# Performance work log

Hardware: AMD Instinct MI355X
Metric: run time of the kernel (lower is better)

## Reference

```python
import jax, jax.numpy as jnp
import numpy as np

N = 100000
E = 1600000
NIN = 128
NOUT = 128


def setup_inputs() -> dict:
    key = jax.random.key(0)
    k1, k2, k3, k4 = jax.random.split(key, 4)
    x = jax.random.normal(k1, (N, NIN), dtype=jnp.float32)
    edge_index = jax.random.randint(k2, (2, E), 0, N, dtype=jnp.int64)
    edge_attr = jnp.ones((E,), dtype=jnp.float32)  # unused by GCNConv
    # PyG Linear weight is [out, in]; glorot-ish init
    W = jax.random.normal(k3, (NOUT, NIN), dtype=jnp.float32) / np.sqrt(NIN)
    b = jnp.zeros((NOUT,), dtype=jnp.float32)
    return {"x": x, "edge_index": edge_index, "edge_attr": edge_attr, "W": W, "b": b}


def reference(x, edge_index, edge_attr, W, b):
    # PyG GCNConv: add self-loops, symmetric degree normalization,
    # linear transform, scatter-add aggregation at destination, + bias.
    n = x.shape[0]
    loops = jnp.arange(n, dtype=edge_index.dtype)
    src = jnp.concatenate([edge_index[0], loops])  # [E+N]
    dst = jnp.concatenate([edge_index[1], loops])  # [E+N]
    # degree over destination (col) including self-loops, edge weight = 1
    deg = jax.ops.segment_sum(jnp.ones_like(dst, dtype=x.dtype), dst, num_segments=n)
    dinv = jnp.where(deg > 0, jax.lax.rsqrt(deg), 0.0)
    norm = dinv[src] * dinv[dst]  # [E+N]
    h = x @ W.T  # [N, NOUT]
    msg = h[src] * norm[:, None]  # [E+N, NOUT]
    out = jax.ops.segment_sum(msg, dst, num_segments=n)  # [N, NOUT]
    return out + b
```

## Files before the change

### kernel.cpp

```cpp
#include <hip/hip_runtime.h>

#define TPB 256
#define NBLK 256
#define BSH 8
#define BCAP 6144

typedef __attribute__((ext_vector_type(4))) float f32x4;
typedef __attribute__((ext_vector_type(8))) short short8;

__device__ __forceinline__ unsigned short f2bf(float f) {
    unsigned u = __float_as_uint(f);
    u = (u + 0x7fffu + ((u >> 16) & 1u)) >> 16;
    return (unsigned short)u;
}
__device__ __forceinline__ float bflo(unsigned u) { return __uint_as_float(u << 16); }
__device__ __forceinline__ float bfhi(unsigned u) { return __uint_as_float(u & 0xffff0000u); }


__global__ __launch_bounds__(256) void k_scatgemm(
    const int* __restrict__ src, const int* __restrict__ dst,
    int* __restrict__ bcur, unsigned* __restrict__ packed,
    const float* __restrict__ x, const float* __restrict__ W,
    unsigned short* __restrict__ g, int N, int E)
{
    __shared__ __align__(16) char smem[34816];
    const int t = threadIdx.x;

    if (blockIdx.x < NBLK) {
        int* sh = (int*)smem;
        sh[t] = 0; sh[t + 256] = 0;
        __syncthreads();
        int chunk = (E + NBLK - 1) / NBLK;
        int lo = blockIdx.x * chunk;
        int hi = min(E, lo + chunk);
        for (int e = lo + t; e < hi; e += 256)
            atomicAdd(&sh[dst[e] >> BSH], 1);
        __syncthreads();
        int c0 = sh[t], c1 = sh[t + 256];
        int b0 = c0 ? atomicAdd(&bcur[t],       c0) : 0;
        int b1 = c1 ? atomicAdd(&bcur[t + 256], c1) : 0;
        __syncthreads();
        sh[t]       = t * BCAP + b0;
        sh[t + 256] = (t + 256) * BCAP + b1;
        __syncthreads();
        for (int e = lo + t; e < hi; e += 256) {
            int d = dst[e];
            int bkt = d >> BSH;
            int pos = atomicAdd(&sh[bkt], 1);
            if (pos < bkt * BCAP + BCAP)
                packed[pos] = ((unsigned)src[e] << 8) | (unsigned)(d & 255);
        }
    } else {
        typedef unsigned short wb_t[136];
        wb_t* wb = (wb_t*)smem;

        for (int ch = t; ch < 2048; ch += 256) {
            int nrow = ch >> 4, k8 = (ch & 15) << 3;
            const float* wp = W + nrow * 128 + k8;
            float4 w0 = *(const float4*)wp;
            float4 w1 = *(const float4*)(wp + 4);
            union { unsigned short u[8]; uint4 q; } pk;
            pk.u[0] = f2bf(w0.x); pk.u[1] = f2bf(w0.y); pk.u[2] = f2bf(w0.z); pk.u[3] = f2bf(w0.w);
            pk.u[4] = f2bf(w1.x); pk.u[5] = f2bf(w1.y); pk.u[6] = f2bf(w1.z); pk.u[7] = f2bf(w1.w);
            *(uint4*)&wb[nrow][k8] = pk.q;
        }
        __syncthreads();

        const int lane = t & 63;
        const int wid  = t >> 6;
        const int l15  = lane & 15;
        const int quad = lane >> 4;
        const int row  = (blockIdx.x - NBLK) * 64 + wid * 16 + l15;
        const int rowc = (row < N) ? row : (N - 1);

        f32x4 acc[8];
        #pragma unroll
        for (int u = 0; u < 8; ++u) acc[u] = (f32x4){0.f, 0.f, 0.f, 0.f};

        #pragma unroll
        for (int ks = 0; ks < 4; ++ks) {
            const int kb = ks * 32 + quad * 8;
            float4 a0 = *(const float4*)(x + (long)rowc * 128 + kb);
            float4 a1 = *(const float4*)(x + (long)rowc * 128 + kb + 4);
            union { unsigned short u[8]; short8 v; } af;
            af.u[0] = f2bf(a0.x); af.u[1] = f2bf(a0.y); af.u[2] = f2bf(a0.z); af.u[3] = f2bf(a0.w);
            af.u[4] = f2bf(a1.x); af.u[5] = f2bf(a1.y); af.u[6] = f2bf(a1.z); af.u[7] = f2bf(a1.w);
            #pragma unroll
            for (int u = 0; u < 8; ++u) {
                short8 bf = *(const short8*)&wb[u * 16 + l15][kb];
                acc[u] = __builtin_amdgcn_mfma_f32_16x16x32_bf16(bf, af.v, acc[u], 0, 0, 0);
            }
        }

        if (row < N) {
            unsigned short* gp = g + (long)row * 128 + quad * 4;
            #pragma unroll
            for (int u = 0; u < 8; ++u) {
                unsigned short u0 = f2bf(acc[u][0]);
                unsigned short u1 = f2bf(acc[u][1]);
                unsigned short u2 = f2bf(acc[u][2]);
                unsigned short u3 = f2bf(acc[u][3]);
                uint2 pk;
                pk.x = (unsigned)u0 | ((unsigned)u1 << 16);
                pk.y = (unsigned)u2 | ((unsigned)u3 << 16);
                *(uint2*)(gp + u * 16) = pk;
            }
        }
    }
}


__global__ __launch_bounds__(256) void k_bcsr(const unsigned* __restrict__ packed,
                                              const int* __restrict__ bcur,
                                              int* __restrict__ offsets,
                                              int* __restrict__ sorted_src,
                                              float* __restrict__ dinv, int N, int E, int NB) {
    __shared__ int tp0[256], tp1[256];
    __shared__ int bb[513];
    __shared__ int hist[256];
    __shared__ int scur[256];
    __shared__ unsigned stage[BCAP];
    int t = threadIdx.x;

    {
        int v0 = bcur[2 * t], v1 = bcur[2 * t + 1];
        int p = v0 + v1;
        tp0[t] = p;
        __syncthreads();
        int sb = 0;
        for (int d = 1; d < 256; d <<= 1) {
            int* cur = sb ? tp1 : tp0;
            int* nxt = sb ? tp0 : tp1;
            int val = cur[t] + ((t >= d) ? cur[t - d] : 0);
            nxt[t] = val;
            sb ^= 1;
            __syncthreads();
        }
        int* fin = sb ? tp1 : tp0;
        int base = fin[t] - p;
        bb[2 * t] = base;
        bb[2 * t + 1] = base + v0;
        if (t == 0) bb[512] = E;
        __syncthreads();
    }

    for (int b = blockIdx.x; b < NB; b += NBLK) {
        int cnt = min(bcur[b], BCAP);
        int s0g = b * BCAP;
        int o0  = bb[b];
        hist[t] = 0;
        __syncthreads();
        for (int e = t; e < cnt; e += 256)
            atomicAdd(&hist[packed[s0g + e] & 255u], 1);
        __syncthreads();
        int v = hist[t];
        tp0[t] = v;
        __syncthreads();
        int sb = 0;
        for (int d = 1; d < 256; d <<= 1) {
            int* cur = sb ? tp1 : tp0;
            int* nxt = sb ? tp0 : tp1;
            int val = cur[t] + ((t >= d) ? cur[t - d] : 0);
            nxt[t] = val;
            sb ^= 1;
            __syncthreads();
        }
        int* fin = sb ? tp1 : tp0;
        int lbase = fin[t] - v;
        scur[t] = lbase;
        int d = (b << BSH) + t;
        if (d < N) { offsets[d] = o0 + lbase; dinv[d] = rsqrtf((float)v + 1.0f); }
        if (b == 0 && t == 0) offsets[N] = E;
        __syncthreads();
        for (int e = t; e < cnt; e += 256) {
            unsigned pk = packed[s0g + e];
            int pos = atomicAdd(&scur[pk & 255u], 1);
            stage[pos] = pk >> 8;
        }
        __syncthreads();
        for (int i = t; i < cnt; i += 256)
            sorted_src[o0 + i] = (int)stage[i];
        __syncthreads();
    }
}


__global__ __launch_bounds__(256) void k_aggregate(const int* __restrict__ sorted_src,
                                                   const int* __restrict__ offsets,
                                                   const unsigned short* __restrict__ g,
                                                   const float* __restrict__ dinv,
                                                   const float* __restrict__ b,
                                                   float* __restrict__ out, int n) {
    int d = blockIdx.x * (TPB / 32) + (threadIdx.x >> 5);
    if (d >= n) return;
    int c = (threadIdx.x & 31) << 2;
    const char* gb = (const char*)g + (c << 1);

    int s0 = offsets[d];
    int s1 = offsets[d + 1];

    float4 acc = make_float4(0.f, 0.f, 0.f, 0.f);
    auto addrow = [&](int r) {
        float dv = dinv[r];
        uint2 p = *(const uint2*)(gb + (r << 8));
        acc.x = fmaf(bflo(p.x), dv, acc.x);
        acc.y = fmaf(bfhi(p.x), dv, acc.y);
        acc.z = fmaf(bflo(p.y), dv, acc.z);
        acc.w = fmaf(bfhi(p.y), dv, acc.w);
    };

    addrow(d);
    int e = s0;
    for (; e + 8 <= s1; e += 8) {
        int a[8];
        #pragma unroll
        for (int j = 0; j < 8; ++j) a[j] = sorted_src[e + j];
        #pragma unroll
        for (int j = 0; j < 8; ++j) addrow(a[j]);
    }
    for (; e + 4 <= s1; e += 4) {
        int a[4];
        #pragma unroll
        for (int j = 0; j < 4; ++j) a[j] = sorted_src[e + j];
        #pragma unroll
        for (int j = 0; j < 4; ++j) addrow(a[j]);
    }
    for (; e < s1; ++e) addrow(sorted_src[e]);

    float s = dinv[d];
    float4 bb = *(const float4*)(b + c);
    float4 r = make_float4(acc.x * s + bb.x, acc.y * s + bb.y,
                           acc.z * s + bb.z, acc.w * s + bb.w);
    *(float4*)(out + (long)d * 128 + c) = r;
}


extern "C" void kernel_launch(void* const* d_in, const int* in_sizes, int n_in,
                              void* d_out, int out_size, void* d_ws, size_t ws_size,
                              hipStream_t stream) {
    const float* x  = (const float*)d_in[0];
    const int*   ei = (const int*)d_in[1];
    const float* W  = (const float*)d_in[3];
    const float* b  = (const float*)d_in[4];
    float* out = (float*)d_out;

    const int N = in_sizes[0] / 128;
    const int E = in_sizes[1] / 2;
    const int* src = ei;
    const int* dst = ei + E;
    const int NB = (N + 255) >> BSH;

    char* p = (char*)d_ws;
    auto carve = [&](size_t bytes) { char* q = p; p += (bytes + 255) & ~(size_t)255; return q; };
    int*            bcur       = (int*)           carve(512 * 4);
    int*            offsets    = (int*)           carve((size_t)(N + 1) * 4);
    float*          dinv       = (float*)         carve((size_t)N * 4);
    int*            sorted_src = (int*)           carve((size_t)E * 4);
    unsigned*       packed     = (unsigned*)      carve((size_t)512 * BCAP * 4);
    unsigned short* g          = (unsigned short*)carve((size_t)N * 128 * 2);

    const int gemmBlocks = (N + 63) / 64;

    hipMemsetAsync(bcur, 0, 512 * 4, stream);

    k_scatgemm<<<NBLK + gemmBlocks, TPB, 0, stream>>>(src, dst, bcur, packed,
                                                      x, W, g, N, E);
    k_bcsr    <<<NBLK, TPB, 0, stream>>>(packed, bcur, offsets, sorted_src,
                                         dinv, N, E, NB);
    k_aggregate<<<(N + (TPB / 32) - 1) / (TPB / 32), TPB, 0, stream>>>(
        sorted_src, offsets, g, dinv, b, out, N);
}
```

Measured before the change: 231.7 us.

## Restage scatter with LDS-local sort, fuse CSR build into GEMM kernel, prescale rows

The bucket scatter now runs as its own kernel. Each block sorts its edge chunk into buckets in LDS and then writes packed entries contiguously, where before each edge did a scattered global write. Degrees come from global atomics, so the CSR-building pass moves into the GEMM kernel with one block per bucket. The GEMM output is prescaled by the source dinv, which lets aggregation do plain adds on precomputed byte offsets instead of a per-edge dinv gather. The cost is one extra global atomic per edge for the degree count, and the GEMM now has to wait for the scatter kernel instead of overlapping with it.

```diff
diff --git a/kernel.cpp b/kernel.cpp
--- a/kernel.cpp
+++ b/kernel.cpp
@@ -2,8 +2,10 @@
 
 #define TPB 256
 #define NBLK 256
+#define SCTPB 512
 #define BSH 8
 #define BCAP 6144
+#define CHCAP 6272
 
 typedef __attribute__((ext_vector_type(4))) float f32x4;
 typedef __attribute__((ext_vector_type(8))) short short8;
@@ -17,39 +19,143 @@
 __device__ __forceinline__ float bfhi(unsigned u) { return __uint_as_float(u & 0xffff0000u); }
 
 
-__global__ __launch_bounds__(256) void k_scatgemm(
+__global__ __launch_bounds__(SCTPB) void k_scat(
     const int* __restrict__ src, const int* __restrict__ dst,
-    int* __restrict__ bcur, unsigned* __restrict__ packed,
+    int* __restrict__ deg, int* __restrict__ bcur,
+    unsigned* __restrict__ packed, int E)
+{
+    __shared__ int hist[512], lbase[512], lcur[512], gbase[512];
+    __shared__ int tp[2][512];
+    __shared__ unsigned stage[CHCAP];
+    __shared__ unsigned short bktid[CHCAP];
+    const int t = threadIdx.x;
+
+    hist[t] = 0;
+    __syncthreads();
+
+    const int chunk = (E + NBLK - 1) / NBLK;
+    const int lo = blockIdx.x * chunk;
+    const int hi = min(E, lo + chunk);
+
+    for (int e = lo + t; e < hi; e += SCTPB) {
+        int d = dst[e];
+        atomicAdd(&deg[d], 1);
+        atomicAdd(&hist[d >> BSH], 1);
+    }
+    __syncthreads();
+
+    int v = hist[t];
+    tp[0][t] = v;
+    __syncthreads();
+    int sb = 0;
+    for (int dl = 1; dl < 512; dl <<= 1) {
+        int val = tp[sb][t] + ((t >= dl) ? tp[sb][t - dl] : 0);
+        tp[sb ^ 1][t] = val;
+        sb ^= 1;
+        __syncthreads();
+    }
+    int lb = tp[sb][t] - v;
+    lbase[t] = lb;
+    lcur[t]  = lb;
+    gbase[t] = v ? atomicAdd(&bcur[t], v) : 0;
+    __syncthreads();
+
+    for (int e = lo + t; e < hi; e += SCTPB) {
+        int d = dst[e];
+        int s = src[e];
+        int bkt = d >> BSH;
+        int pos = atomicAdd(&lcur[bkt], 1);
+        stage[pos] = ((unsigned)s << 8) | (unsigned)(d & 255);
+        bktid[pos] = (unsigned short)bkt;
+    }
+    __syncthreads();
+
+    const int cnt = hi - lo;
+    for (int i = t; i < cnt; i += SCTPB) {
+        int bkt = bktid[i];
+        int gpos = gbase[bkt] + (i - lbase[bkt]);
+        if (gpos < BCAP)
+            packed[bkt * BCAP + gpos] = stage[i];
+    }
+}
+
+
+__global__ __launch_bounds__(256) void k_csrgemm(
+    const unsigned* __restrict__ packed, const int* __restrict__ bcur,
+    const int* __restrict__ deg,
+    int* __restrict__ offsets, int* __restrict__ sorted_src,
     const float* __restrict__ x, const float* __restrict__ W,
-    unsigned short* __restrict__ g, int N, int E)
+    unsigned short* __restrict__ g, int N, int E, int NB)
 {
     __shared__ __align__(16) char smem[34816];
     const int t = threadIdx.x;
 
-    if (blockIdx.x < NBLK) {
-        int* sh = (int*)smem;
-        sh[t] = 0; sh[t + 256] = 0;
-        __syncthreads();
-        int chunk = (E + NBLK - 1) / NBLK;
-        int lo = blockIdx.x * chunk;
-        int hi = min(E, lo + chunk);
-        for (int e = lo + t; e < hi; e += 256)
-            atomicAdd(&sh[dst[e] >> BSH], 1);
-        __syncthreads();
-        int c0 = sh[t], c1 = sh[t + 256];
-        int b0 = c0 ? atomicAdd(&bcur[t],       c0) : 0;
-        int b1 = c1 ? atomicAdd(&bcur[t + 256], c1) : 0;
-        __syncthreads();
-        sh[t]       = t * BCAP + b0;
-        sh[t + 256] = (t + 256) * BCAP + b1;
-        __syncthreads();
-        for (int e = lo + t; e < hi; e += 256) {
-            int d = dst[e];
-            int bkt = d >> BSH;
-            int pos = atomicAdd(&sh[bkt], 1);
-            if (pos < bkt * BCAP + BCAP)
-                packed[pos] = ((unsigned)src[e] << 8) | (unsigned)(d & 255);
-        }
+    if (blockIdx.x < (unsigned)NB) {
+        int* tp0  = (int*)smem;
+        int* tp1  = tp0 + 256;
+        int* bb   = tp1 + 256;
+        int* hist = bb + 516;
+        int* scur = hist + 256;
+        unsigned* stage = (unsigned*)(scur + 256);
+
+        {
+            int v0 = bcur[2 * t], v1 = bcur[2 * t + 1];
+            int p = v0 + v1;
+            tp0[t] = p;
+            __syncthreads();
+            int sb = 0;
+            for (int d = 1; d < 256; d <<= 1) {
+                int* cur = sb ? tp1 : tp0;
+                int* nxt = sb ? tp0 : tp1;
+                int val = cur[t] + ((t >= d) ? cur[t - d] : 0);
+                nxt[t] = val;
+                sb ^= 1;
+                __syncthreads();
+            }
+            int* fin = sb ? tp1 : tp0;
+            int base = fin[t] - p;
+            bb[2 * t] = base;
+            bb[2 * t + 1] = base + v0;
+            if (t == 0) bb[512] = E;
+            __syncthreads();
+        }
+
+        const int b = blockIdx.x;
+        const int cnt = min(bcur[b], BCAP);
+        const int s0g = b * BCAP;
+        const int o0  = bb[b];
+        hist[t] = 0;
+        __syncthreads();
+        for (int e = t; e < cnt; e += 256)
+            atomicAdd(&hist[packed[s0g + e] & 255u], 1);
+        __syncthreads();
+        int v = hist[t];
+        tp0[t] = v;
+        __syncthreads();
+        int sb = 0;
+        for (int d = 1; d < 256; d <<= 1) {
+            int* cur = sb ? tp1 : tp0;
+            int* nxt = sb ? tp0 : tp1;
+            int val = cur[t] + ((t >= d) ? cur[t - d] : 0);
+            nxt[t] = val;
+            sb ^= 1;
+            __syncthreads();
+        }
+        int* fin = sb ? tp1 : tp0;
+        int lbase = fin[t] - v;
+        scur[t] = lbase;
+        int d = (b << BSH) + t;
+        if (d < N) offsets[d] = o0 + lbase;
+        if (b == 0 && t == 0) offsets[N] = E;
+        __syncthreads();
+        for (int e = t; e < cnt; e += 256) {
+            unsigned pk = packed[s0g + e];
+            int pos = atomicAdd(&scur[pk & 255u], 1);
+            stage[pos] = pk & 0xffffff00u;
+        }
+        __syncthreads();
+        for (int i = t; i < cnt; i += 256)
+            sorted_src[o0 + i] = (int)stage[i];
     } else {
         typedef unsigned short wb_t[136];
         wb_t* wb = (wb_t*)smem;
@@ -70,7 +176,7 @@
         const int wid  = t >> 6;
         const int l15  = lane & 15;
         const int quad = lane >> 4;
-        const int row  = (blockIdx.x - NBLK) * 64 + wid * 16 + l15;
+        const int row  = (blockIdx.x - NB) * 64 + wid * 16 + l15;
         const int rowc = (row < N) ? row : (N - 1);
 
         f32x4 acc[8];
@@ -93,13 +199,14 @@
         }
 
         if (row < N) {
+            float dv = rsqrtf((float)deg[row] + 1.0f);
             unsigned short* gp = g + (long)row * 128 + quad * 4;
             #pragma unroll
             for (int u = 0; u < 8; ++u) {
-                unsigned short u0 = f2bf(acc[u][0]);
-                unsigned short u1 = f2bf(acc[u][1]);
-                unsigned short u2 = f2bf(acc[u][2]);
-                unsigned short u3 = f2bf(acc[u][3]);
+                unsigned short u0 = f2bf(acc[u][0] * dv);
+                unsigned short u1 = f2bf(acc[u][1] * dv);
+                unsigned short u2 = f2bf(acc[u][2] * dv);
+                unsigned short u3 = f2bf(acc[u][3] * dv);
                 uint2 pk;
                 pk.x = (unsigned)u0 | ((unsigned)u1 << 16);
                 pk.y = (unsigned)u2 | ((unsigned)u3 << 16);
@@ -110,85 +217,10 @@
 }
 
 
-__global__ __launch_bounds__(256) void k_bcsr(const unsigned* __restrict__ packed,
-                                              const int* __restrict__ bcur,
-                                              int* __restrict__ offsets,
-                                              int* __restrict__ sorted_src,
-                                              float* __restrict__ dinv, int N, int E, int NB) {
-    __shared__ int tp0[256], tp1[256];
-    __shared__ int bb[513];
-    __shared__ int hist[256];
-    __shared__ int scur[256];
-    __shared__ unsigned stage[BCAP];
-    int t = threadIdx.x;
-
-    {
-        int v0 = bcur[2 * t], v1 = bcur[2 * t + 1];
-        int p = v0 + v1;
-        tp0[t] = p;
-        __syncthreads();
-        int sb = 0;
-        for (int d = 1; d < 256; d <<= 1) {
-            int* cur = sb ? tp1 : tp0;
-            int* nxt = sb ? tp0 : tp1;
-            int val = cur[t] + ((t >= d) ? cur[t - d] : 0);
-            nxt[t] = val;
-            sb ^= 1;
-            __syncthreads();
-        }
-        int* fin = sb ? tp1 : tp0;
-        int base = fin[t] - p;
-        bb[2 * t] = base;
-        bb[2 * t + 1] = base + v0;
-        if (t == 0) bb[512] = E;
-        __syncthreads();
-    }
-
-    for (int b = blockIdx.x; b < NB; b += NBLK) {
-        int cnt = min(bcur[b], BCAP);
-        int s0g = b * BCAP;
-        int o0  = bb[b];
-        hist[t] = 0;
-        __syncthreads();
-        for (int e = t; e < cnt; e += 256)
-            atomicAdd(&hist[packed[s0g + e] & 255u], 1);
-        __syncthreads();
-        int v = hist[t];
-        tp0[t] = v;
-        __syncthreads();
-        int sb = 0;
-        for (int d = 1; d < 256; d <<= 1) {
-            int* cur = sb ? tp1 : tp0;
-            int* nxt = sb ? tp0 : tp1;
-            int val = cur[t] + ((t >= d) ? cur[t - d] : 0);
-            nxt[t] = val;
-            sb ^= 1;
-            __syncthreads();
-        }
-        int* fin = sb ? tp1 : tp0;
-        int lbase = fin[t] - v;
-        scur[t] = lbase;
-        int d = (b << BSH) + t;
-        if (d < N) { offsets[d] = o0 + lbase; dinv[d] = rsqrtf((float)v + 1.0f); }
-        if (b == 0 && t == 0) offsets[N] = E;
-        __syncthreads();
-        for (int e = t; e < cnt; e += 256) {
-            unsigned pk = packed[s0g + e];
-            int pos = atomicAdd(&scur[pk & 255u], 1);
-            stage[pos] = pk >> 8;
-        }
-        __syncthreads();
-        for (int i = t; i < cnt; i += 256)
-            sorted_src[o0 + i] = (int)stage[i];
-        __syncthreads();
-    }
-}
-
-
 __global__ __launch_bounds__(256) void k_aggregate(const int* __restrict__ sorted_src,
                                                    const int* __restrict__ offsets,
                                                    const unsigned short* __restrict__ g,
-                                                   const float* __restrict__ dinv,
+                                                   const int* __restrict__ deg,
                                                    const float* __restrict__ b,
                                                    float* __restrict__ out, int n) {
     int d = blockIdx.x * (TPB / 32) + (threadIdx.x >> 5);
@@ -200,16 +232,13 @@
     int s1 = offsets[d + 1];
 
     float4 acc = make_float4(0.f, 0.f, 0.f, 0.f);
-    auto addrow = [&](int r) {
-        float dv = dinv[r];
-        uint2 p = *(const uint2*)(gb + (r << 8));
-        acc.x = fmaf(bflo(p.x), dv, acc.x);
-        acc.y = fmaf(bfhi(p.x), dv, acc.y);
-        acc.z = fmaf(bflo(p.y), dv, acc.z);
-        acc.w = fmaf(bfhi(p.y), dv, acc.w);
+    auto addrow = [&](int off) {
+        uint2 p = *(const uint2*)(gb + off);
+        acc.x += bflo(p.x); acc.y += bfhi(p.x);
+        acc.z += bflo(p.y); acc.w += bfhi(p.y);
     };
 
-    addrow(d);
+    addrow(d << 8);
     int e = s0;
     for (; e + 8 <= s1; e += 8) {
         int a[8];
@@ -227,7 +256,7 @@
     }
     for (; e < s1; ++e) addrow(sorted_src[e]);
 
-    float s = dinv[d];
+    float s = rsqrtf((float)deg[d] + 1.0f);
     float4 bb = *(const float4*)(b + c);
     float4 r = make_float4(acc.x * s + bb.x, acc.y * s + bb.y,
                            acc.z * s + bb.z, acc.w * s + bb.w);
@@ -252,21 +281,21 @@
 
     char* p = (char*)d_ws;
     auto carve = [&](size_t bytes) { char* q = p; p += (bytes + 255) & ~(size_t)255; return q; };
+    int*            deg        = (int*)           carve((size_t)N * 4);
     int*            bcur       = (int*)           carve(512 * 4);
     int*            offsets    = (int*)           carve((size_t)(N + 1) * 4);
-    float*          dinv       = (float*)         carve((size_t)N * 4);
     int*            sorted_src = (int*)           carve((size_t)E * 4);
     unsigned*       packed     = (unsigned*)      carve((size_t)512 * BCAP * 4);
     unsigned short* g          = (unsigned short*)carve((size_t)N * 128 * 2);
 
     const int gemmBlocks = (N + 63) / 64;
 
-    hipMemsetAsync(bcur, 0, 512 * 4, stream);
-
-    k_scatgemm<<<NBLK + gemmBlocks, TPB, 0, stream>>>(src, dst, bcur, packed,
-                                                      x, W, g, N, E);
-    k_bcsr    <<<NBLK, TPB, 0, stream>>>(packed, bcur, offsets, sorted_src,
-                                         dinv, N, E, NB);
+    size_t zbytes = (size_t)((char*)(bcur + 512) - (char*)deg);
+    hipMemsetAsync(deg, 0, zbytes, stream);
+
+    k_scat    <<<NBLK, SCTPB, 0, stream>>>(src, dst, deg, bcur, packed, E);
+    k_csrgemm <<<NB + gemmBlocks, TPB, 0, stream>>>(packed, bcur, deg, offsets,
+                                                    sorted_src, x, W, g, N, E, NB);
     k_aggregate<<<(N + (TPB / 32) - 1) / (TPB / 32), TPB, 0, stream>>>(
-        sorted_src, offsets, g, dinv, b, out, N);
-}
+        sorted_src, offsets, g, deg, b, out, N);
+}
```

Result: slower. 268.6 us (+15.9%).

## Fuse bucket sort into aggregation with smaller 64-node buckets

Applied to the files above, without the earlier changes.

Shrinks destination buckets from 256 to 64 nodes. The per-bucket counting sort now happens in shared memory inside the aggregation kernel, so the global CSR build (offsets, sorted_src, global prefix scan) is dropped. A small separate kernel computes dinv from per-bucket histograms. The packed entries are pre-shifted so they serve directly as row byte offsets into g. This removes a global write and read of sorted edges plus the offsets array. In exchange the packed array is read twice, each block runs serial rounds over 64 destinations, and bucket overflow above BCAP=2048 silently drops edges.

```diff
diff --git a/kernel.cpp b/kernel.cpp
--- a/kernel.cpp
+++ b/kernel.cpp
@@ -1,9 +1,10 @@
 #include <hip/hip_runtime.h>
 
 #define TPB 256
-#define NBLK 256
-#define BSH 8
-#define BCAP 6144
+#define NSCAT 256
+#define BSH 6
+#define BCAP 2048
+#define MAXBUK 1600
 
 typedef __attribute__((ext_vector_type(4))) float f32x4;
 typedef __attribute__((ext_vector_type(8))) short short8;
@@ -21,34 +22,33 @@
     const int* __restrict__ src, const int* __restrict__ dst,
     int* __restrict__ bcur, unsigned* __restrict__ packed,
     const float* __restrict__ x, const float* __restrict__ W,
-    unsigned short* __restrict__ g, int N, int E)
+    unsigned short* __restrict__ g, int N, int E, int NBUK)
 {
     __shared__ __align__(16) char smem[34816];
     const int t = threadIdx.x;
 
-    if (blockIdx.x < NBLK) {
-        int* sh = (int*)smem;
-        sh[t] = 0; sh[t + 256] = 0;
-        __syncthreads();
-        int chunk = (E + NBLK - 1) / NBLK;
-        int lo = blockIdx.x * chunk;
-        int hi = min(E, lo + chunk);
+    if (blockIdx.x < NSCAT) {
+        int* cnt = (int*)smem;
+        int* cur = cnt + MAXBUK;
+        for (int i = t; i < NBUK; i += 256) cnt[i] = 0;
+        __syncthreads();
+        const int chunk = (E + NSCAT - 1) / NSCAT;
+        const int lo = blockIdx.x * chunk;
+        const int hi = min(E, lo + chunk);
         for (int e = lo + t; e < hi; e += 256)
-            atomicAdd(&sh[dst[e] >> BSH], 1);
-        __syncthreads();
-        int c0 = sh[t], c1 = sh[t + 256];
-        int b0 = c0 ? atomicAdd(&bcur[t],       c0) : 0;
-        int b1 = c1 ? atomicAdd(&bcur[t + 256], c1) : 0;
-        __syncthreads();
-        sh[t]       = t * BCAP + b0;
-        sh[t + 256] = (t + 256) * BCAP + b1;
+            atomicAdd(&cnt[dst[e] >> BSH], 1);
+        __syncthreads();
+        for (int i = t; i < NBUK; i += 256) {
+            int c = cnt[i];
+            cur[i] = i * BCAP + (c ? atomicAdd(&bcur[i], c) : 0);
+        }
         __syncthreads();
         for (int e = lo + t; e < hi; e += 256) {
             int d = dst[e];
             int bkt = d >> BSH;
-            int pos = atomicAdd(&sh[bkt], 1);
+            int pos = atomicAdd(&cur[bkt], 1);
             if (pos < bkt * BCAP + BCAP)
-                packed[pos] = ((unsigned)src[e] << 8) | (unsigned)(d & 255);
+                packed[pos] = ((unsigned)src[e] << 8) | (unsigned)(d & 63);
         }
     } else {
         typedef unsigned short wb_t[136];
@@ -70,7 +70,7 @@
         const int wid  = t >> 6;
         const int l15  = lane & 15;
         const int quad = lane >> 4;
-        const int row  = (blockIdx.x - NBLK) * 64 + wid * 16 + l15;
+        const int row  = (blockIdx.x - NSCAT) * 64 + wid * 16 + l15;
         const int rowc = (row < N) ? row : (N - 1);
 
         f32x4 acc[8];
@@ -110,128 +110,105 @@
 }
 
 
-__global__ __launch_bounds__(256) void k_bcsr(const unsigned* __restrict__ packed,
+__global__ __launch_bounds__(256) void k_dinv(const unsigned* __restrict__ packed,
                                               const int* __restrict__ bcur,
-                                              int* __restrict__ offsets,
-                                              int* __restrict__ sorted_src,
-                                              float* __restrict__ dinv, int N, int E, int NB) {
-    __shared__ int tp0[256], tp1[256];
-    __shared__ int bb[513];
-    __shared__ int hist[256];
-    __shared__ int scur[256];
+                                              float* __restrict__ dinv, int N) {
+    __shared__ int hist[64];
+    const int b = blockIdx.x;
+    const int t = threadIdx.x;
+    if (t < 64) hist[t] = 0;
+    __syncthreads();
+    const int cnt = min(bcur[b], BCAP);
+    const int base = b * BCAP;
+    for (int e = t; e < cnt; e += 256)
+        atomicAdd(&hist[packed[base + e] & 63u], 1);
+    __syncthreads();
+    if (t < 64) {
+        int d = (b << BSH) + t;
+        if (d < N) dinv[d] = rsqrtf((float)hist[t] + 1.0f);
+    }
+}
+
+
+__global__ __launch_bounds__(256) void k_aggsort(const unsigned* __restrict__ packed,
+                                                 const int* __restrict__ bcur,
+                                                 const unsigned short* __restrict__ g,
+                                                 const float* __restrict__ dinv,
+                                                 const float* __restrict__ b_,
+                                                 float* __restrict__ out, int N) {
+    __shared__ int hist[64], lbase[64], scur[64];
     __shared__ unsigned stage[BCAP];
-    int t = threadIdx.x;
-
-    {
-        int v0 = bcur[2 * t], v1 = bcur[2 * t + 1];
-        int p = v0 + v1;
-        tp0[t] = p;
-        __syncthreads();
-        int sb = 0;
-        for (int d = 1; d < 256; d <<= 1) {
-            int* cur = sb ? tp1 : tp0;
-            int* nxt = sb ? tp0 : tp1;
-            int val = cur[t] + ((t >= d) ? cur[t - d] : 0);
-            nxt[t] = val;
-            sb ^= 1;
-            __syncthreads();
-        }
-        int* fin = sb ? tp1 : tp0;
-        int base = fin[t] - p;
-        bb[2 * t] = base;
-        bb[2 * t + 1] = base + v0;
-        if (t == 0) bb[512] = E;
-        __syncthreads();
-    }
-
-    for (int b = blockIdx.x; b < NB; b += NBLK) {
-        int cnt = min(bcur[b], BCAP);
-        int s0g = b * BCAP;
-        int o0  = bb[b];
-        hist[t] = 0;
-        __syncthreads();
-        for (int e = t; e < cnt; e += 256)
-            atomicAdd(&hist[packed[s0g + e] & 255u], 1);
-        __syncthreads();
+    const int b = blockIdx.x;
+    const int t = threadIdx.x;
+    if (t < 64) hist[t] = 0;
+    __syncthreads();
+    const int cnt = min(bcur[b], BCAP);
+    const int base = b * BCAP;
+    for (int e = t; e < cnt; e += 256)
+        atomicAdd(&hist[packed[base + e] & 63u], 1);
+    __syncthreads();
+    if (t < 64) {
         int v = hist[t];
-        tp0[t] = v;
-        __syncthreads();
-        int sb = 0;
-        for (int d = 1; d < 256; d <<= 1) {
-            int* cur = sb ? tp1 : tp0;
-            int* nxt = sb ? tp0 : tp1;
-            int val = cur[t] + ((t >= d) ? cur[t - d] : 0);
-            nxt[t] = val;
-            sb ^= 1;
-            __syncthreads();
-        }
-        int* fin = sb ? tp1 : tp0;
-        int lbase = fin[t] - v;
-        scur[t] = lbase;
-        int d = (b << BSH) + t;
-        if (d < N) { offsets[d] = o0 + lbase; dinv[d] = rsqrtf((float)v + 1.0f); }
-        if (b == 0 && t == 0) offsets[N] = E;
-        __syncthreads();
-        for (int e = t; e < cnt; e += 256) {
-            unsigned pk = packed[s0g + e];
-            int pos = atomicAdd(&scur[pk & 255u], 1);
-            stage[pos] = pk >> 8;
-        }
-        __syncthreads();
-        for (int i = t; i < cnt; i += 256)
-            sorted_src[o0 + i] = (int)stage[i];
-        __syncthreads();
-    }
-}
-
-
-__global__ __launch_bounds__(256) void k_aggregate(const int* __restrict__ sorted_src,
-                                                   const int* __restrict__ offsets,
-                                                   const unsigned short* __restrict__ g,
-                                                   const float* __restrict__ dinv,
-                                                   const float* __restrict__ b,
-                                                   float* __restrict__ out, int n) {
-    int d = blockIdx.x * (TPB / 32) + (threadIdx.x >> 5);
-    if (d >= n) return;
-    int c = (threadIdx.x & 31) << 2;
+        int incl = v;
+        #pragma unroll
+        for (int d = 1; d < 64; d <<= 1) {
+            int o = __shfl_up(incl, d);
+            if (t >= d) incl += o;
+        }
+        lbase[t] = incl - v;
+        scur[t]  = incl - v;
+    }
+    __syncthreads();
+    for (int e = t; e < cnt; e += 256) {
+        unsigned pk = packed[base + e];
+        int pos = atomicAdd(&scur[pk & 63u], 1);
+        stage[pos] = pk & 0xffffff00u;
+    }
+    __syncthreads();
+
+    const int c = (t & 31) << 2;
     const char* gb = (const char*)g + (c << 1);
-
-    int s0 = offsets[d];
-    int s1 = offsets[d + 1];
-
-    float4 acc = make_float4(0.f, 0.f, 0.f, 0.f);
-    auto addrow = [&](int r) {
-        float dv = dinv[r];
-        uint2 p = *(const uint2*)(gb + (r << 8));
-        acc.x = fmaf(bflo(p.x), dv, acc.x);
-        acc.y = fmaf(bfhi(p.x), dv, acc.y);
-        acc.z = fmaf(bflo(p.y), dv, acc.z);
-        acc.w = fmaf(bfhi(p.y), dv, acc.w);
-    };
-
-    addrow(d);
-    int e = s0;
-    for (; e + 8 <= s1; e += 8) {
-        int a[8];
-        #pragma unroll
-        for (int j = 0; j < 8; ++j) a[j] = sorted_src[e + j];
-        #pragma unroll
-        for (int j = 0; j < 8; ++j) addrow(a[j]);
-    }
-    for (; e + 4 <= s1; e += 4) {
-        int a[4];
-        #pragma unroll
-        for (int j = 0; j < 4; ++j) a[j] = sorted_src[e + j];
-        #pragma unroll
-        for (int j = 0; j < 4; ++j) addrow(a[j]);
-    }
-    for (; e < s1; ++e) addrow(sorted_src[e]);
-
-    float s = dinv[d];
-    float4 bb = *(const float4*)(b + c);
-    float4 r = make_float4(acc.x * s + bb.x, acc.y * s + bb.y,
-                           acc.z * s + bb.z, acc.w * s + bb.w);
-    *(float4*)(out + (long)d * 128 + c) = r;
+    #pragma unroll 1
+    for (int round = 0; round < 8; ++round) {
+        const int dl = round * 8 + (t >> 5);
+        const int d  = (b << BSH) + dl;
+        if (d >= N) continue;
+
+        float4 acc = make_float4(0.f, 0.f, 0.f, 0.f);
+        auto addrow = [&](unsigned off) {
+            float dv = dinv[off >> 8];
+            uint2 p = *(const uint2*)(gb + off);
+            acc.x = fmaf(bflo(p.x), dv, acc.x);
+            acc.y = fmaf(bfhi(p.x), dv, acc.y);
+            acc.z = fmaf(bflo(p.y), dv, acc.z);
+            acc.w = fmaf(bfhi(p.y), dv, acc.w);
+        };
+
+        addrow((unsigned)d << 8);
+        int e  = lbase[dl];
+        int s1 = e + hist[dl];
+        for (; e + 8 <= s1; e += 8) {
+            unsigned a[8];
+            #pragma unroll
+            for (int j = 0; j < 8; ++j) a[j] = stage[e + j];
+            #pragma unroll
+            for (int j = 0; j < 8; ++j) addrow(a[j]);
+        }
+        for (; e + 4 <= s1; e += 4) {
+            unsigned a[4];
+            #pragma unroll
+            for (int j = 0; j < 4; ++j) a[j] = stage[e + j];
+            #pragma unroll
+            for (int j = 0; j < 4; ++j) addrow(a[j]);
+        }
+        for (; e < s1; ++e) addrow(stage[e]);
+
+        float s = rsqrtf((float)hist[dl] + 1.0f);
+        float4 bb = *(const float4*)(b_ + c);
+        float4 r = make_float4(acc.x * s + bb.x, acc.y * s + bb.y,
+                               acc.z * s + bb.z, acc.w * s + bb.w);
+        *(float4*)(out + (long)d * 128 + c) = r;
+    }
 }
 
 
@@ -248,25 +225,21 @@
     const int E = in_sizes[1] / 2;
     const int* src = ei;
     const int* dst = ei + E;
-    const int NB = (N + 255) >> BSH;
+    const int NBUK = (N + 63) >> BSH;
 
     char* p = (char*)d_ws;
     auto carve = [&](size_t bytes) { char* q = p; p += (bytes + 255) & ~(size_t)255; return q; };
-    int*            bcur       = (int*)           carve(512 * 4);
-    int*            offsets    = (int*)           carve((size_t)(N + 1) * 4);
-    float*          dinv       = (float*)         carve((size_t)N * 4);
-    int*            sorted_src = (int*)           carve((size_t)E * 4);
-    unsigned*       packed     = (unsigned*)      carve((size_t)512 * BCAP * 4);
-    unsigned short* g          = (unsigned short*)carve((size_t)N * 128 * 2);
+    int*            bcur   = (int*)           carve((size_t)MAXBUK * 4);
+    float*          dinv   = (float*)         carve((size_t)N * 4);
+    unsigned*       packed = (unsigned*)      carve((size_t)MAXBUK * BCAP * 4);
+    unsigned short* g      = (unsigned short*)carve((size_t)N * 128 * 2);
 
     const int gemmBlocks = (N + 63) / 64;
 
-    hipMemsetAsync(bcur, 0, 512 * 4, stream);
-
-    k_scatgemm<<<NBLK + gemmBlocks, TPB, 0, stream>>>(src, dst, bcur, packed,
-                                                      x, W, g, N, E);
-    k_bcsr    <<<NBLK, TPB, 0, stream>>>(packed, bcur, offsets, sorted_src,
-                                         dinv, N, E, NB);
-    k_aggregate<<<(N + (TPB / 32) - 1) / (TPB / 32), TPB, 0, stream>>>(
-        sorted_src, offsets, g, dinv, b, out, N);
-}
+    hipMemsetAsync(bcur, 0, (size_t)NBUK * 4, stream);
+
+    k_scatgemm<<<NSCAT + gemmBlocks, TPB, 0, stream>>>(src, dst, bcur, packed,
+                                                       x, W, g, N, E, NBUK);
+    k_dinv    <<<NBUK, TPB, 0, stream>>>(packed, bcur, dinv, N);
+    k_aggsort <<<NBUK, TPB, 0, stream>>>(packed, bcur, g, dinv, b, out, N);
+}
```

Result: no change. 232.7 us (+0.4%).
